# Kernel optimization log

Hardware: AMD Instinct MI355X
Metric: run time of the kernel (lower is better)

Reference implementation:

```python
import jax, jax.numpy as jnp
import numpy as np

T, B, CIN, V = 4, 16, 2, 128
E, H, DEPTH, NC = 512, 8, 6, 11
HID = 4 * E
TAU = 2.0
EPS = 1e-5
ALPHA = 4.0  # sigmoid surrogate width (spikingjelly default)


@jax.custom_vjp
def spike(x):
    return (x >= 0.0).astype(x.dtype)

def _spike_fwd(x):
    return spike(x), x

def _spike_bwd(x, g):
    s = jax.nn.sigmoid(ALPHA * x)
    return (g * ALPHA * s * (1.0 - s),)

spike.defvjp(_spike_fwd, _spike_bwd)


def lif(x, vth):
    # x: [T, ...]; LIF with decay_input=True, v_reset=0 (hard reset)
    def step(v, xt):
        v = v + (xt - v) / TAU
        s = spike(v - vth)
        return v * (1.0 - s), s
    return jax.lax.scan(step, jnp.zeros_like(x[0]), x)[1]


def bn(x, p):
    # x: [T,B,C,V], p: [4,C] = (gamma, beta, mean, var); inference-mode BN
    g, b, m, v = p
    inv = g / jnp.sqrt(v + EPS)
    return (x - m[:, None]) * inv[:, None] + b[:, None]


def conv1x1(x, w):
    # kernel-size-1 Conv1d == channel matmul
    return jnp.einsum('tbcv,oc->tbov', x, w)


def attention(x, w, bnp):
    # w: [4,C,C] (q,k,v,proj); bnp: [4,2,4,C] (RepConv bn + extra bn)
    t, b_, C, v_ = x.shape
    c = C // H
    h = lif(x, 1.0)

    def branch(i):
        return bn(bn(conv1x1(h, w[i]), bnp[i, 0]), bnp[i, 1])

    def heads(z):  # [T,B,C,V] -> [T,B,H,N,c], channel split heads-major
        return z.reshape(t, b_, H, c, v_).transpose(0, 1, 2, 4, 3)

    q = heads(lif(branch(0), 1.0))
    k = heads(lif(branch(1), 1.0))
    vv = heads(lif(branch(2), 1.0))
    kv = jnp.einsum('tbhnc,tbhnd->tbhcd', k, vv)      # linear attention: k^T v
    o = jnp.einsum('tbhnc,tbhcd->tbhnd', q, kv) * 0.125
    o = o.transpose(0, 1, 2, 4, 3).reshape(t, b_, C, v_)
    a = lif(o, 0.5)
    return bn(bn(conv1x1(a, w[3]), bnp[3, 0]), bnp[3, 1])


def mlp(x, w1, b1, p1, w2, b2, p2):
    h = lif(x, 1.0)
    h = bn(conv1x1(h, w1) + b1[:, None], p1)
    h = lif(h, 1.0)
    return bn(conv1x1(h, w2) + b2[:, None], p2)


def _mk_bn(key, lead, c):
    k1, k2, k3, k4 = jax.random.split(key, 4)
    g = 1.0 + 0.1 * jax.random.normal(k1, (*lead, c))
    b = 0.1 * jax.random.normal(k2, (*lead, c))
    m = 0.1 * jax.random.normal(k3, (*lead, c))
    v = jax.random.uniform(k4, (*lead, c), minval=0.5, maxval=1.5)
    return jnp.stack([g, b, m, v], axis=-2)


def setup_inputs() -> dict:
    key = jax.random.key(0)
    ks = jax.random.split(key, 16)
    std = 0.02
    return {
        'x': jax.random.normal(ks[0], (T, B, CIN, V), dtype=jnp.float32),
        'pe_w': std * jax.random.normal(ks[1], (E, CIN)),
        'pe_bn': _mk_bn(ks[2], (), E),
        'qkvp_w': std * jax.random.normal(ks[3], (DEPTH, 4, E, E)),
        'qkvp_bn': _mk_bn(ks[4], (DEPTH, 4, 2), E),
        'fc1_w': std * jax.random.normal(ks[5], (DEPTH, HID, E)),
        'fc1_b': jnp.zeros((DEPTH, HID)),
        'fc1_bn': _mk_bn(ks[6], (DEPTH,), HID),
        'fc2_w': std * jax.random.normal(ks[7], (DEPTH, E, HID)),
        'fc2_b': jnp.zeros((DEPTH, E)),
        'fc2_bn': _mk_bn(ks[8], (DEPTH,), E),
        'head_w': std * jax.random.normal(ks[9], (NC, E)),
        'head_b': jnp.zeros((NC,)),
    }


def reference(x, pe_w, pe_bn, qkvp_w, qkvp_bn, fc1_w, fc1_b, fc1_bn,
              fc2_w, fc2_b, fc2_bn, head_w, head_b):
    # patch embed (first layer: no LIF)
    h = bn(conv1x1(x, pe_w), pe_bn)
    for d in range(DEPTH):
        h = h + attention(h, qkvp_w[d], qkvp_bn[d])
        h = h + mlp(h, fc1_w[d], fc1_b[d], fc1_bn[d], fc2_w[d], fc2_b[d], fc2_bn[d])
    h = h.mean(axis=3)          # [T,B,E]
    s = lif(h, 1.0)             # head_lif
    out = (s @ head_w.T + head_b).mean(axis=0)  # [B,NC]
    return out
```

## Files before the change

kernel.cpp:

```cpp
#include <hip/hip_runtime.h>

#define TT 4
#define BB 16
#define VV 128
#define EE 512
#define HIDC 2048
#define BN_EPS 1e-5f

typedef unsigned int u32;
typedef unsigned long long u64;
typedef unsigned short u16;

__global__ __launch_bounds__(256) void trans_all(const float* __restrict__ qw,
    const float* __restrict__ f1w, const float* __restrict__ f2w,
    float* __restrict__ wq, float* __restrict__ w1, float* __restrict__ w2)
{
  const int d = blockIdx.z, zz = blockIdx.y;
  const float* src; float* dst; int O, C;
  if (zz < 4)      { src = qw + ((size_t)d * 4 + zz) * EE * EE; dst = wq + ((size_t)d * 4 + zz) * EE * EE; O = EE; C = EE; }
  else if (zz == 4){ src = f1w + (size_t)d * HIDC * EE; dst = w1 + (size_t)d * HIDC * EE; O = HIDC; C = EE; }
  else             { src = f2w + (size_t)d * EE * HIDC; dst = w2 + (size_t)d * EE * HIDC; O = EE; C = HIDC; }
  const int tc_n = C >> 5, to_n = O >> 5;
  const int bx = blockIdx.x;
  if (bx >= tc_n * to_n) return;
  const int tc = bx % tc_n, to = bx / tc_n;
  __shared__ float t[32][33];
  const int tx = threadIdx.x & 31, ty = threadIdx.x >> 5;
#pragma unroll
  for (int k = 0; k < 4; ++k) {
    int o = to * 32 + ty + k * 8, c = tc * 32 + tx;
    t[ty + k * 8][tx] = src[(size_t)o * C + c];
  }
  __syncthreads();
#pragma unroll
  for (int k = 0; k < 4; ++k) {
    int c = tc * 32 + ty + k * 8, o = to * 32 + tx;
    dst[(size_t)c * O + o] = t[tx][ty + k * 8];
  }
}

__global__ __launch_bounds__(256) void pe_lif(const float* __restrict__ x,
    const float* __restrict__ w, const float* __restrict__ bnp,
    float* __restrict__ h, u32* __restrict__ mIn)
{
  const int g = blockIdx.x * 4 + (threadIdx.x >> 6);
  const int lane = threadIdx.x & 63;
  const int b = g >> 9, e = g & 511;
  const float w0 = w[e * 2], w1 = w[e * 2 + 1];
  const float gg = bnp[e], be = bnp[EE + e], mm = bnp[2 * EE + e], vr = bnp[3 * EE + e];
  const float sc = gg / sqrtf(vr + BN_EPS);
  float v0 = 0.f, v1 = 0.f;
#pragma unroll
  for (int t = 0; t < TT; ++t) {
    const int tb = t * BB + b;
    const float* xb = x + (size_t)tb * 2 * VV;
    float a0 = (w0 * xb[lane]      + w1 * xb[VV + lane]      - mm) * sc + be;
    float a1 = (w0 * xb[lane + 64] + w1 * xb[VV + lane + 64] - mm) * sc + be;
    size_t o = ((size_t)tb * EE + e) * VV + lane;
    h[o] = a0; h[o + 64] = a1;
    v0 += (a0 - v0) * 0.5f; v1 += (a1 - v1) * 0.5f;
    float s0 = (v0 >= 1.f) ? 1.f : 0.f, s1 = (v1 >= 1.f) ? 1.f : 0.f;
    v0 *= (1.f - s0); v1 *= (1.f - s1);
    u64 m0 = __ballot(s0 != 0.f);
    u64 m1 = __ballot(s1 != 0.f);
    if (lane == 0) {
      uint4 mw = {(u32)m0, (u32)(m0 >> 32), (u32)m1, (u32)(m1 >> 32)};
      *(uint4*)&mIn[((size_t)tb * EE + e) * 4] = mw;
    }
  }
}

__global__ __launch_bounds__(256) void gemm_fused(
    const u32* __restrict__ InM, const float* __restrict__ WT,
    float* __restrict__ OutPre, const float* __restrict__ resid,
    u32* __restrict__ SpkM, const float* __restrict__ bias,
    const float* __restrict__ bn1, const float* __restrict__ bn2,
    int C, int O, float vth, long wtZ, long spkZ, long bnZ)
{
  const int b = blockIdx.x, ob = blockIdx.y * 16, z = blockIdx.z;
  const int tid = threadIdx.x, lane = tid & 63, wv = tid >> 6;
  WT += (long)z * wtZ; SpkM += (long)z * spkZ;
  if (bn1) bn1 += (long)z * bnZ;
  if (bn2) bn2 += (long)z * bnZ;

  __shared__ float sW[16][16];
  __shared__ u32 sM[16][4];
  __shared__ u16 slist[2048];
  __shared__ u32 wsum[4], woff[4], runb;

  const int og = (tid >> 5) * 2;
  const bool hasb = (bias != nullptr), has1 = (bn1 != nullptr), has2 = (bn2 != nullptr);

  float bs[2], m1c[2], s1c[2], b1c[2], m2c[2], s2c[2], b2c[2];
#pragma unroll
  for (int j = 0; j < 2; ++j) {
    int o = ob + og + j;
    bs[j] = hasb ? bias[o] : 0.f;
    if (has1) { float g = bn1[o]; b1c[j] = bn1[O + o]; m1c[j] = bn1[2 * O + o];
                s1c[j] = g / sqrtf(bn1[3 * O + o] + BN_EPS); }
    if (has2) { float g = bn2[o]; b2c[j] = bn2[O + o]; m2c[j] = bn2[2 * O + o];
                s2c[j] = g / sqrtf(bn2[3 * O + o] + BN_EPS); }
  }

  float st[2][4] = {};

  for (int t = 0; t < TT; ++t) {
    const u32* Mrow = InM + (size_t)(t * BB + b) * C * 4;
    __syncthreads();
    if (tid == 0) runb = 0;
    __syncthreads();
    for (int c0 = 0; c0 < C; c0 += 256) {
      uint4 r = *(const uint4*)&Mrow[(size_t)(c0 + tid) * 4];
      bool f = (r.x | r.y | r.z | r.w) != 0;
      u64 m = __ballot(f);
      if (lane == 0) wsum[wv] = __popcll(m);
      __syncthreads();
      if (tid == 0) { u32 s = runb;
#pragma unroll
        for (int k = 0; k < 4; ++k) { woff[k] = s; s += wsum[k]; } runb = s; }
      __syncthreads();
      if (f) { int rank = __popcll(m & ((1ull << lane) - 1));
               slist[woff[wv] + rank] = (u16)(c0 + tid); }
      __syncthreads();
    }
    const int n = (int)runb;

    float acc[2][4] = {};
    int a0 = 0;
    while (a0 < n) {
      int m = n - a0; if (m > 16) m = 16;
      if (tid < 64) {
        int cc = tid >> 2, q = tid & 3;
        if (cc < m) {
          int c = slist[a0 + cc];
          sM[cc][q] = Mrow[(size_t)c * 4 + q];
          *(float4*)&sW[cc][q * 4] = *(const float4*)&WT[(size_t)c * O + ob + q * 4];
        }
      }
      __syncthreads();
#pragma unroll 4
      for (int cc = 0; cc < m; ++cc) {
        u32 mw = sM[cc][(tid & 31) >> 3];
        u32 nib = mw >> ((tid & 7) * 4);
        float2 w2 = *(const float2*)&sW[cc][og];
        float i0 = (nib & 1u) ? 1.f : 0.f;
        float i1 = (nib & 2u) ? 1.f : 0.f;
        float i2 = (nib & 4u) ? 1.f : 0.f;
        float i3 = (nib & 8u) ? 1.f : 0.f;
        acc[0][0] += w2.x * i0; acc[0][1] += w2.x * i1;
        acc[0][2] += w2.x * i2; acc[0][3] += w2.x * i3;
        acc[1][0] += w2.y * i0; acc[1][1] += w2.y * i1;
        acc[1][2] += w2.y * i2; acc[1][3] += w2.y * i3;
      }
      __syncthreads();
      a0 += 16;
    }

#pragma unroll
    for (int j = 0; j < 2; ++j) {
      float a[4] = {acc[j][0], acc[j][1], acc[j][2], acc[j][3]};
      if (hasb) {
#pragma unroll
        for (int k = 0; k < 4; ++k) a[k] += bs[j];
      }
      if (has1) {
#pragma unroll
        for (int k = 0; k < 4; ++k) a[k] = (a[k] - m1c[j]) * s1c[j] + b1c[j];
      }
      if (has2) {
#pragma unroll
        for (int k = 0; k < 4; ++k) a[k] = (a[k] - m2c[j]) * s2c[j] + b2c[j];
      }
      size_t orow = (size_t)(t * BB + b) * O + ob + og + j;
      if (OutPre) {
        size_t oi = orow * VV + (tid & 31) * 4;
        float4 r = *(const float4*)&resid[oi];
        a[0] += r.x; a[1] += r.y; a[2] += r.z; a[3] += r.w;
        float4 wr = {a[0], a[1], a[2], a[3]};
        *(float4*)&OutPre[oi] = wr;
      }
      u32 nib = 0;
#pragma unroll
      for (int k = 0; k < 4; ++k) {
        st[j][k] += (a[k] - st[j][k]) * 0.5f;
        float sp = (st[j][k] >= vth) ? 1.f : 0.f;
        st[j][k] *= (1.f - sp);
        nib |= (sp != 0.f) ? (1u << k) : 0u;
      }
      u32 wmask = nib << ((tid & 7) * 4);
      wmask |= __shfl_xor(wmask, 1);
      wmask |= __shfl_xor(wmask, 2);
      wmask |= __shfl_xor(wmask, 4);
      if ((tid & 7) == 0) SpkM[orow * 4 + ((tid & 31) >> 3)] = wmask;
    }
  }
}

__global__ __launch_bounds__(256) void attn_fused(const u32* __restrict__ Qm,
    const u32* __restrict__ Km, const u32* __restrict__ Vm, u32* __restrict__ Om)
{
  const int b = blockIdx.x, hh = blockIdx.y, dh = blockIdx.z;
  const int tid = threadIdx.x, lane = tid & 63;
  __shared__ float sQ[64][132];
  __shared__ float sKV[64][36];
  __shared__ u64 sKm[64][2], sQm[64][2], sVm[32][2];
  __shared__ u32 sQnz[64];
  const int np = lane * 2;
  const int dg = (tid >> 6) * 8;
  float st[8][2] = {};
  for (int t = 0; t < TT; ++t) {
    const int tb = t * BB + b;
    __syncthreads();
    if (tid < 64) {
      uint4 q = *(const uint4*)&Qm[((size_t)tb * EE + hh * 64 + tid) * 4];
      sQm[tid][0] = ((u64)q.y << 32) | q.x; sQm[tid][1] = ((u64)q.w << 32) | q.z;
      sQnz[tid] = q.x | q.y | q.z | q.w;
      uint4 k = *(const uint4*)&Km[((size_t)tb * EE + hh * 64 + tid) * 4];
      sKm[tid][0] = ((u64)k.y << 32) | k.x; sKm[tid][1] = ((u64)k.w << 32) | k.z;
    } else if (tid < 96) {
      int d = tid - 64;
      uint4 v = *(const uint4*)&Vm[((size_t)tb * EE + hh * 64 + dh * 32 + d) * 4];
      sVm[d][0] = ((u64)v.y << 32) | v.x; sVm[d][1] = ((u64)v.w << 32) | v.z;
    }
    __syncthreads();
    {
      int c = tid >> 2, dq = (tid & 3) * 8;
      u64 k0 = sKm[c][0], k1 = sKm[c][1];
#pragma unroll
      for (int i = 0; i < 8; ++i) {
        int d = dq + i;
        int p = __popcll(k0 & sVm[d][0]) + __popcll(k1 & sVm[d][1]);
        sKV[c][d] = (float)p;
      }
    }
    {
      int c = tid >> 2, nq = (tid & 3) * 32;
      u64 qw = sQm[c][nq >> 6] >> (nq & 32);
#pragma unroll
      for (int kk = 0; kk < 8; ++kk) {
        float4 f = {(qw >> (kk * 4)) & 1 ? 1.f : 0.f,
                    (qw >> (kk * 4 + 1)) & 1 ? 1.f : 0.f,
                    (qw >> (kk * 4 + 2)) & 1 ? 1.f : 0.f,
                    (qw >> (kk * 4 + 3)) & 1 ? 1.f : 0.f};
        *(float4*)&sQ[c][nq + kk * 4] = f;
      }
    }
    __syncthreads();
    float acc[8][2] = {};
    for (int c = 0; c < 64; ++c) {
      if (!sQnz[c]) continue;
      float2 q2 = *(const float2*)&sQ[c][np];
      float4 wa = *(const float4*)&sKV[c][dg];
      float4 wb = *(const float4*)&sKV[c][dg + 4];
      float w8[8] = {wa.x, wa.y, wa.z, wa.w, wb.x, wb.y, wb.z, wb.w};
#pragma unroll
      for (int i = 0; i < 8; ++i) { acc[i][0] += w8[i] * q2.x; acc[i][1] += w8[i] * q2.y; }
    }
#pragma unroll
    for (int i = 0; i < 8; ++i) {
      float a0 = acc[i][0] * 0.125f, a1 = acc[i][1] * 0.125f;
      st[i][0] += (a0 - st[i][0]) * 0.5f; st[i][1] += (a1 - st[i][1]) * 0.5f;
      float s0 = (st[i][0] >= 0.5f) ? 1.f : 0.f, s1 = (st[i][1] >= 0.5f) ? 1.f : 0.f;
      st[i][0] *= (1.f - s0); st[i][1] *= (1.f - s1);
      u32 two = ((s0 != 0.f) ? 1u : 0u) | ((s1 != 0.f) ? 2u : 0u);
      u32 wmask = two << ((lane & 15) * 2);
      wmask |= __shfl_xor(wmask, 1);
      wmask |= __shfl_xor(wmask, 2);
      wmask |= __shfl_xor(wmask, 4);
      wmask |= __shfl_xor(wmask, 8);
      if ((lane & 15) == 0)
        Om[((size_t)tb * EE + hh * 64 + dh * 32 + dg + i) * 4 + (lane >> 4)] = wmask;
    }
  }
}

__global__ __launch_bounds__(256) void mean_lif(const float* __restrict__ h,
    float* __restrict__ sh)
{
  int i = blockIdx.x * 256 + threadIdx.x;
  float v = 0.f;
#pragma unroll
  for (int t = 0; t < TT; ++t) {
    const float* p = h + ((size_t)t * BB * EE + i) * VV;
    float s = 0.f;
#pragma unroll
    for (int q = 0; q < VV; q += 4) {
      float4 x = *(const float4*)&p[q];
      s += x.x + x.y + x.z + x.w;
    }
    float hm = s * (1.f / 128.f);
    v += (hm - v) * 0.5f;
    float sp = (v >= 1.f) ? 1.f : 0.f;
    sh[(size_t)t * (BB * EE) + i] = sp;
    v *= (1.f - sp);
  }
}

__global__ __launch_bounds__(256) void head_k2(const float* __restrict__ sh,
    const float* __restrict__ hw, const float* __restrict__ hb,
    float* __restrict__ out)
{
  int g = blockIdx.x * 4 + (threadIdx.x >> 6);
  int lane = threadIdx.x & 63;
  if (g >= BB * 11) return;
  int b = g / 11, n = g % 11;
  float s = 0.f;
#pragma unroll
  for (int t = 0; t < TT; ++t) {
    const float* sp = sh + (size_t)t * (BB * EE) + b * EE;
    const float* wp = hw + n * EE;
    float ss = 0.f;
#pragma unroll
    for (int e = 0; e < EE; e += 64) ss += sp[e + lane] * wp[e + lane];
#pragma unroll
    for (int off = 32; off; off >>= 1) ss += __shfl_down(ss, off);
    if (lane == 0) s += ss;
  }
  if (lane == 0) out[g] = s * 0.25f + hb[n];
}

extern "C" void kernel_launch(void* const* d_in, const int* in_sizes, int n_in,
                              void* d_out, int out_size, void* d_ws, size_t ws_size,
                              hipStream_t stream) {
  const float* x       = (const float*)d_in[0];
  const float* pe_w    = (const float*)d_in[1];
  const float* pe_bn   = (const float*)d_in[2];
  const float* qkvp_w  = (const float*)d_in[3];
  const float* qkvp_bn = (const float*)d_in[4];
  const float* fc1_w   = (const float*)d_in[5];
  const float* fc1_b   = (const float*)d_in[6];
  const float* fc1_bn  = (const float*)d_in[7];
  const float* fc2_w   = (const float*)d_in[8];
  const float* fc2_b   = (const float*)d_in[9];
  const float* fc2_bn  = (const float*)d_in[10];
  const float* head_w  = (const float*)d_in[11];
  const float* head_b  = (const float*)d_in[12];
  float* out = (float*)d_out;

  const size_t NH = (size_t)TT * BB * EE * VV;
  float* ws = (float*)d_ws;
  float* h   = ws;
  float* wq  = h + NH;
  float* w1  = wq + (size_t)6 * 4 * EE * EE;
  float* w2  = w1 + (size_t)6 * HIDC * EE;
  float* sh  = w2 + (size_t)6 * EE * HIDC;
  u32* mIn  = (u32*)(sh + (size_t)TT * BB * EE);
  u32* mQKV = mIn + (size_t)64 * EE * 4;
  u32* mO   = mQKV + (size_t)3 * 64 * EE * 4;
  u32* mMlp = mO + (size_t)64 * EE * 4;
  u32* mHid = mMlp + (size_t)64 * EE * 4;

  u32* mQ = mQKV;
  u32* mK = mQKV + (size_t)64 * EE * 4;
  u32* mV = mQKV + (size_t)2 * 64 * EE * 4;

  trans_all<<<dim3(1024, 6, 6), 256, 0, stream>>>(qkvp_w, fc1_w, fc2_w, wq, w1, w2);
  pe_lif<<<BB * EE / 4, 256, 0, stream>>>(x, pe_w, pe_bn, h, mIn);

  for (int d = 0; d < 6; ++d) {
    const float* bn1p = qkvp_bn + (size_t)d * 4 * 2 * 4 * EE;
    gemm_fused<<<dim3(BB, EE / 16, 3), 256, 0, stream>>>(mIn,
        wq + (size_t)d * 4 * EE * EE, nullptr, nullptr, mQ, nullptr,
        bn1p, bn1p + 4 * EE, EE, EE, 1.f,
        (long)EE * EE, (long)64 * EE * 4, (long)2 * 4 * EE);
    attn_fused<<<dim3(BB, 8, 2), 256, 0, stream>>>(mQ, mK, mV, mO);
    gemm_fused<<<dim3(BB, EE / 16, 1), 256, 0, stream>>>(mO,
        wq + ((size_t)d * 4 + 3) * EE * EE, h, h, mMlp, nullptr,
        bn1p + 3 * (2 * 4 * EE), bn1p + 3 * (2 * 4 * EE) + 4 * EE,
        EE, EE, 1.f, 0, 0, 0);
    gemm_fused<<<dim3(BB, HIDC / 16, 1), 256, 0, stream>>>(mMlp,
        w1 + (size_t)d * HIDC * EE, nullptr, nullptr, mHid,
        fc1_b + (size_t)d * HIDC, fc1_bn + (size_t)d * 4 * HIDC, nullptr,
        EE, HIDC, 1.f, 0, 0, 0);
    gemm_fused<<<dim3(BB, EE / 16, 1), 256, 0, stream>>>(mHid,
        w2 + (size_t)d * EE * HIDC, h, h, mIn,
        fc2_b + (size_t)d * EE, fc2_bn + (size_t)d * 4 * EE, nullptr,
        HIDC, EE, 1.f, 0, 0, 0);
  }

  mean_lif<<<32, 256, 0, stream>>>(h, sh);
  head_k2<<<44, 256, 0, stream>>>(sh, head_w, head_b, out);
}
```

Before: 602.9 us.

## Emit sparse active-channel lists from producers and load weights directly in GEMM

Producers of spike masks (patch embed, attention, GEMM epilogues) now also write per-16-channel-block counts and lists of channels with any spike, so the consumer GEMM no longer scans all input masks with ballots and barriers to build its list. The GEMM inner loop drops the shared-memory staging of weights and masks and reads them straight from global memory per active channel, removing two barriers per chunk. It adds serial single-thread list building in producers, extra global traffic for counts and ids, and uncoalesced per-thread weight loads that rely on caches.

```diff
diff --git a/kernel.cpp b/kernel.cpp
--- a/kernel.cpp
+++ b/kernel.cpp
@@ -10,6 +10,7 @@
 typedef unsigned int u32;
 typedef unsigned long long u64;
 typedef unsigned short u16;
+typedef unsigned char u8;
 
 __global__ __launch_bounds__(256) void trans_all(const float* __restrict__ qw,
     const float* __restrict__ f1w, const float* __restrict__ f2w,
@@ -41,52 +42,77 @@
 
 __global__ __launch_bounds__(256) void pe_lif(const float* __restrict__ x,
     const float* __restrict__ w, const float* __restrict__ bnp,
-    float* __restrict__ h, u32* __restrict__ mIn)
-{
-  const int g = blockIdx.x * 4 + (threadIdx.x >> 6);
-  const int lane = threadIdx.x & 63;
-  const int b = g >> 9, e = g & 511;
+    float* __restrict__ h, u32* __restrict__ mIn,
+    u32* __restrict__ cnt, u16* __restrict__ ids)
+{
+  const int b = blockIdx.x, eb = blockIdx.y;
+  const int tid = threadIdx.x;
+  const int chl = tid >> 4, e = eb * 16 + chl;
+  const int vs = (tid & 15) * 8;
+  __shared__ u8 sB[16][16];
+  __shared__ u8 sAct[16];
   const float w0 = w[e * 2], w1 = w[e * 2 + 1];
   const float gg = bnp[e], be = bnp[EE + e], mm = bnp[2 * EE + e], vr = bnp[3 * EE + e];
   const float sc = gg / sqrtf(vr + BN_EPS);
-  float v0 = 0.f, v1 = 0.f;
-#pragma unroll
+  float vm[8];
+#pragma unroll
+  for (int k = 0; k < 8; ++k) vm[k] = 0.f;
   for (int t = 0; t < TT; ++t) {
     const int tb = t * BB + b;
-    const float* xb = x + (size_t)tb * 2 * VV;
-    float a0 = (w0 * xb[lane]      + w1 * xb[VV + lane]      - mm) * sc + be;
-    float a1 = (w0 * xb[lane + 64] + w1 * xb[VV + lane + 64] - mm) * sc + be;
-    size_t o = ((size_t)tb * EE + e) * VV + lane;
-    h[o] = a0; h[o + 64] = a1;
-    v0 += (a0 - v0) * 0.5f; v1 += (a1 - v1) * 0.5f;
-    float s0 = (v0 >= 1.f) ? 1.f : 0.f, s1 = (v1 >= 1.f) ? 1.f : 0.f;
-    v0 *= (1.f - s0); v1 *= (1.f - s1);
-    u64 m0 = __ballot(s0 != 0.f);
-    u64 m1 = __ballot(s1 != 0.f);
-    if (lane == 0) {
-      uint4 mw = {(u32)m0, (u32)(m0 >> 32), (u32)m1, (u32)(m1 >> 32)};
-      *(uint4*)&mIn[((size_t)tb * EE + e) * 4] = mw;
-    }
+    const float* xb = x + (size_t)tb * 2 * VV + vs;
+    float4 x0a = *(const float4*)&xb[0],   x0b = *(const float4*)&xb[4];
+    float4 x1a = *(const float4*)&xb[VV],  x1b = *(const float4*)&xb[VV + 4];
+    float a[8] = {x0a.x, x0a.y, x0a.z, x0a.w, x0b.x, x0b.y, x0b.z, x0b.w};
+    float c1[8] = {x1a.x, x1a.y, x1a.z, x1a.w, x1b.x, x1b.y, x1b.z, x1b.w};
+    u32 byte = 0;
+#pragma unroll
+    for (int k = 0; k < 8; ++k) {
+      a[k] = (w0 * a[k] + w1 * c1[k] - mm) * sc + be;
+      vm[k] += (a[k] - vm[k]) * 0.5f;
+      float sp = (vm[k] >= 1.f) ? 1.f : 0.f;
+      vm[k] *= (1.f - sp);
+      byte |= (sp != 0.f) ? (1u << k) : 0u;
+    }
+    size_t ho = ((size_t)tb * EE + e) * VV + vs;
+    float4 ha = {a[0], a[1], a[2], a[3]}, hb = {a[4], a[5], a[6], a[7]};
+    *(float4*)&h[ho] = ha; *(float4*)&h[ho + 4] = hb;
+    sB[chl][tid & 15] = (u8)byte;
+    __syncthreads();
+    if (tid < 16) {
+      uint4 mw = *(const uint4*)&sB[tid][0];
+      *(uint4*)&mIn[((size_t)tb * EE + eb * 16 + tid) * 4] = mw;
+      sAct[tid] = (mw.x | mw.y | mw.z | mw.w) ? 1 : 0;
+    }
+    __syncthreads();
+    if (tid == 0) {
+      int c = 0;
+      for (int i = 0; i < 16; ++i)
+        if (sAct[i]) ids[((size_t)tb * 32 + eb) * 16 + c++] = (u16)(eb * 16 + i);
+      cnt[(size_t)tb * 32 + eb] = c;
+    }
+    __syncthreads();
   }
 }
 
 __global__ __launch_bounds__(256) void gemm_fused(
-    const u32* __restrict__ InM, const float* __restrict__ WT,
-    float* __restrict__ OutPre, const float* __restrict__ resid,
-    u32* __restrict__ SpkM, const float* __restrict__ bias,
-    const float* __restrict__ bn1, const float* __restrict__ bn2,
+    const u32* __restrict__ InM, const u32* __restrict__ cntI,
+    const u16* __restrict__ idsI, int nblkI,
+    const float* __restrict__ WT, float* __restrict__ OutPre,
+    const float* __restrict__ resid, u32* __restrict__ SpkM,
+    u32* __restrict__ cntO, u16* __restrict__ idsO,
+    const float* __restrict__ bias, const float* __restrict__ bn1,
+    const float* __restrict__ bn2,
     int C, int O, float vth, long wtZ, long spkZ, long bnZ)
 {
   const int b = blockIdx.x, ob = blockIdx.y * 16, z = blockIdx.z;
-  const int tid = threadIdx.x, lane = tid & 63, wv = tid >> 6;
+  const int tid = threadIdx.x;
   WT += (long)z * wtZ; SpkM += (long)z * spkZ;
   if (bn1) bn1 += (long)z * bnZ;
   if (bn2) bn2 += (long)z * bnZ;
 
-  __shared__ float sW[16][16];
-  __shared__ u32 sM[16][4];
   __shared__ u16 slist[2048];
-  __shared__ u32 wsum[4], woff[4], runb;
+  __shared__ u32 scnt[128], soff[128], runb;
+  __shared__ u8 sAct[16];
 
   const int og = (tid >> 5) * 2;
   const bool hasb = (bias != nullptr), has1 = (bn1 != nullptr), has2 = (bn2 != nullptr);
@@ -105,55 +131,42 @@
   float st[2][4] = {};
 
   for (int t = 0; t < TT; ++t) {
-    const u32* Mrow = InM + (size_t)(t * BB + b) * C * 4;
-    __syncthreads();
-    if (tid == 0) runb = 0;
-    __syncthreads();
-    for (int c0 = 0; c0 < C; c0 += 256) {
-      uint4 r = *(const uint4*)&Mrow[(size_t)(c0 + tid) * 4];
-      bool f = (r.x | r.y | r.z | r.w) != 0;
-      u64 m = __ballot(f);
-      if (lane == 0) wsum[wv] = __popcll(m);
-      __syncthreads();
-      if (tid == 0) { u32 s = runb;
-#pragma unroll
-        for (int k = 0; k < 4; ++k) { woff[k] = s; s += wsum[k]; } runb = s; }
-      __syncthreads();
-      if (f) { int rank = __popcll(m & ((1ull << lane) - 1));
-               slist[woff[wv] + rank] = (u16)(c0 + tid); }
-      __syncthreads();
-    }
+    const int tb = t * BB + b;
+    __syncthreads();
+    if (tid < nblkI) scnt[tid] = cntI[(size_t)tb * nblkI + tid];
+    __syncthreads();
+    if (tid == 0) {
+      u32 s = 0;
+      for (int i = 0; i < nblkI; ++i) { soff[i] = s; s += scnt[i]; }
+      runb = s;
+    }
+    __syncthreads();
+    if (tid < nblkI) {
+      u32 o = soff[tid], cn = scnt[tid];
+      const u16* src = idsI + ((size_t)tb * nblkI + tid) * 16;
+      for (u32 k = 0; k < cn; ++k) slist[o + k] = src[k];
+    }
+    __syncthreads();
     const int n = (int)runb;
 
     float acc[2][4] = {};
-    int a0 = 0;
-    while (a0 < n) {
-      int m = n - a0; if (m > 16) m = 16;
-      if (tid < 64) {
-        int cc = tid >> 2, q = tid & 3;
-        if (cc < m) {
-          int c = slist[a0 + cc];
-          sM[cc][q] = Mrow[(size_t)c * 4 + q];
-          *(float4*)&sW[cc][q * 4] = *(const float4*)&WT[(size_t)c * O + ob + q * 4];
-        }
-      }
-      __syncthreads();
+    const u32* Mb = InM + (size_t)tb * C * 4 + ((tid & 31) >> 3);
+    const float* Wb = WT + ob + og;
+    const int sh4 = (tid & 7) * 4;
 #pragma unroll 4
-      for (int cc = 0; cc < m; ++cc) {
-        u32 mw = sM[cc][(tid & 31) >> 3];
-        u32 nib = mw >> ((tid & 7) * 4);
-        float2 w2 = *(const float2*)&sW[cc][og];
-        float i0 = (nib & 1u) ? 1.f : 0.f;
-        float i1 = (nib & 2u) ? 1.f : 0.f;
-        float i2 = (nib & 4u) ? 1.f : 0.f;
-        float i3 = (nib & 8u) ? 1.f : 0.f;
-        acc[0][0] += w2.x * i0; acc[0][1] += w2.x * i1;
-        acc[0][2] += w2.x * i2; acc[0][3] += w2.x * i3;
-        acc[1][0] += w2.y * i0; acc[1][1] += w2.y * i1;
-        acc[1][2] += w2.y * i2; acc[1][3] += w2.y * i3;
-      }
-      __syncthreads();
-      a0 += 16;
+    for (int i = 0; i < n; ++i) {
+      int c = slist[i];
+      u32 mw = Mb[(size_t)c * 4];
+      float2 w2 = *(const float2*)&Wb[(size_t)c * O];
+      u32 nib = mw >> sh4;
+      float i0 = (nib & 1u) ? 1.f : 0.f;
+      float i1 = (nib & 2u) ? 1.f : 0.f;
+      float i2 = (nib & 4u) ? 1.f : 0.f;
+      float i3 = (nib & 8u) ? 1.f : 0.f;
+      acc[0][0] += w2.x * i0; acc[0][1] += w2.x * i1;
+      acc[0][2] += w2.x * i2; acc[0][3] += w2.x * i3;
+      acc[1][0] += w2.y * i0; acc[1][1] += w2.y * i1;
+      acc[1][2] += w2.y * i2; acc[1][3] += w2.y * i3;
     }
 
 #pragma unroll
@@ -171,7 +184,7 @@
 #pragma unroll
         for (int k = 0; k < 4; ++k) a[k] = (a[k] - m2c[j]) * s2c[j] + b2c[j];
       }
-      size_t orow = (size_t)(t * BB + b) * O + ob + og + j;
+      size_t orow = (size_t)tb * O + ob + og + j;
       if (OutPre) {
         size_t oi = orow * VV + (tid & 31) * 4;
         float4 r = *(const float4*)&resid[oi];
@@ -187,17 +200,30 @@
         st[j][k] *= (1.f - sp);
         nib |= (sp != 0.f) ? (1u << k) : 0u;
       }
-      u32 wmask = nib << ((tid & 7) * 4);
+      u32 wmask = nib << sh4;
       wmask |= __shfl_xor(wmask, 1);
       wmask |= __shfl_xor(wmask, 2);
       wmask |= __shfl_xor(wmask, 4);
       if ((tid & 7) == 0) SpkM[orow * 4 + ((tid & 31) >> 3)] = wmask;
+      u32 aw = wmask | __shfl_xor(wmask, 8);
+      aw |= __shfl_xor(aw, 16);
+      if ((tid & 31) == 0) sAct[(tid >> 5) * 2 + j] = aw ? 1 : 0;
+    }
+    if (cntO) {
+      __syncthreads();
+      if (tid == 0) {
+        int c = 0;
+        for (int i = 0; i < 16; ++i)
+          if (sAct[i]) idsO[((size_t)tb * gridDim.y + blockIdx.y) * 16 + c++] = (u16)(ob + i);
+        cntO[(size_t)tb * gridDim.y + blockIdx.y] = c;
+      }
     }
   }
 }
 
 __global__ __launch_bounds__(256) void attn_fused(const u32* __restrict__ Qm,
-    const u32* __restrict__ Km, const u32* __restrict__ Vm, u32* __restrict__ Om)
+    const u32* __restrict__ Km, const u32* __restrict__ Vm, u32* __restrict__ Om,
+    u32* __restrict__ cntO, u16* __restrict__ idsO)
 {
   const int b = blockIdx.x, hh = blockIdx.y, dh = blockIdx.z;
   const int tid = threadIdx.x, lane = tid & 63;
@@ -205,6 +231,7 @@
   __shared__ float sKV[64][36];
   __shared__ u64 sKm[64][2], sQm[64][2], sVm[32][2];
   __shared__ u32 sQnz[64];
+  __shared__ u8 sAct[32];
   const int np = lane * 2;
   const int dg = (tid >> 6) * 8;
   float st[8][2] = {};
@@ -270,6 +297,18 @@
       wmask |= __shfl_xor(wmask, 8);
       if ((lane & 15) == 0)
         Om[((size_t)tb * EE + hh * 64 + dh * 32 + dg + i) * 4 + (lane >> 4)] = wmask;
+      u32 aw = wmask | __shfl_xor(wmask, 16);
+      aw |= __shfl_xor(aw, 32);
+      if (lane == 0) sAct[dg + i] = aw ? 1 : 0;
+    }
+    __syncthreads();
+    if (tid < 2) {
+      int slot = hh * 4 + dh * 2 + tid;
+      int c = 0;
+      for (int i = 0; i < 16; ++i)
+        if (sAct[tid * 16 + i])
+          idsO[((size_t)tb * 32 + slot) * 16 + c++] = (u16)(hh * 64 + dh * 32 + tid * 16 + i);
+      cntO[(size_t)tb * 32 + slot] = c;
     }
   }
 }
@@ -349,31 +388,39 @@
   u32* mO   = mQKV + (size_t)3 * 64 * EE * 4;
   u32* mMlp = mO + (size_t)64 * EE * 4;
   u32* mHid = mMlp + (size_t)64 * EE * 4;
+  u32* cntIn = mHid + (size_t)64 * HIDC * 4;
+  u32* cntO  = cntIn + 64 * 32;
+  u32* cntM  = cntO + 64 * 32;
+  u32* cntH  = cntM + 64 * 32;
+  u16* idsIn = (u16*)(cntH + 64 * 128);
+  u16* idsO  = idsIn + (size_t)64 * 32 * 16;
+  u16* idsM  = idsO + (size_t)64 * 32 * 16;
+  u16* idsH  = idsM + (size_t)64 * 32 * 16;
 
   u32* mQ = mQKV;
   u32* mK = mQKV + (size_t)64 * EE * 4;
   u32* mV = mQKV + (size_t)2 * 64 * EE * 4;
 
   trans_all<<<dim3(1024, 6, 6), 256, 0, stream>>>(qkvp_w, fc1_w, fc2_w, wq, w1, w2);
-  pe_lif<<<BB * EE / 4, 256, 0, stream>>>(x, pe_w, pe_bn, h, mIn);
+  pe_lif<<<dim3(BB, EE / 16), 256, 0, stream>>>(x, pe_w, pe_bn, h, mIn, cntIn, idsIn);
 
   for (int d = 0; d < 6; ++d) {
     const float* bn1p = qkvp_bn + (size_t)d * 4 * 2 * 4 * EE;
-    gemm_fused<<<dim3(BB, EE / 16, 3), 256, 0, stream>>>(mIn,
-        wq + (size_t)d * 4 * EE * EE, nullptr, nullptr, mQ, nullptr,
-        bn1p, bn1p + 4 * EE, EE, EE, 1.f,
+    gemm_fused<<<dim3(BB, EE / 16, 3), 256, 0, stream>>>(mIn, cntIn, idsIn, 32,
+        wq + (size_t)d * 4 * EE * EE, nullptr, nullptr, mQ, nullptr, nullptr,
+        nullptr, bn1p, bn1p + 4 * EE, EE, EE, 1.f,
         (long)EE * EE, (long)64 * EE * 4, (long)2 * 4 * EE);
-    attn_fused<<<dim3(BB, 8, 2), 256, 0, stream>>>(mQ, mK, mV, mO);
-    gemm_fused<<<dim3(BB, EE / 16, 1), 256, 0, stream>>>(mO,
-        wq + ((size_t)d * 4 + 3) * EE * EE, h, h, mMlp, nullptr,
-        bn1p + 3 * (2 * 4 * EE), bn1p + 3 * (2 * 4 * EE) + 4 * EE,
+    attn_fused<<<dim3(BB, 8, 2), 256, 0, stream>>>(mQ, mK, mV, mO, cntO, idsO);
+    gemm_fused<<<dim3(BB, EE / 16, 1), 256, 0, stream>>>(mO, cntO, idsO, 32,
+        wq + ((size_t)d * 4 + 3) * EE * EE, h, h, mMlp, cntM, idsM,
+        nullptr, bn1p + 3 * (2 * 4 * EE), bn1p + 3 * (2 * 4 * EE) + 4 * EE,
         EE, EE, 1.f, 0, 0, 0);
-    gemm_fused<<<dim3(BB, HIDC / 16, 1), 256, 0, stream>>>(mMlp,
-        w1 + (size_t)d * HIDC * EE, nullptr, nullptr, mHid,
+    gemm_fused<<<dim3(BB, HIDC / 16, 1), 256, 0, stream>>>(mMlp, cntM, idsM, 32,
+        w1 + (size_t)d * HIDC * EE, nullptr, nullptr, mHid, cntH, idsH,
         fc1_b + (size_t)d * HIDC, fc1_bn + (size_t)d * 4 * HIDC, nullptr,
         EE, HIDC, 1.f, 0, 0, 0);
-    gemm_fused<<<dim3(BB, EE / 16, 1), 256, 0, stream>>>(mHid,
-        w2 + (size_t)d * EE * HIDC, h, h, mIn,
+    gemm_fused<<<dim3(BB, EE / 16, 1), 256, 0, stream>>>(mHid, cntH, idsH, 128,
+        w2 + (size_t)d * EE * HIDC, h, h, mIn, cntIn, idsIn,
         fc2_b + (size_t)d * EE, fc2_bn + (size_t)d * 4 * EE, nullptr,
         HIDC, EE, 1.f, 0, 0, 0);
   }
```

Measured after the change: 791.9 us. +31.3%, slower.
